# Kernel optimization log

Hardware: AMD Instinct MI355X
Metric: run time of the kernel (lower is better)

The kernel has to match this reference:

```python
import jax, jax.numpy as jnp
import numpy as np

GRID_SIZE = 2
AREA_SPAN = 1.6
EPS = 0.01
N = 4096
HIDDEN = 64
NUM_SCENES = 64


def setup_inputs() -> dict:
    key = jax.random.key(0)
    k1, k2, k3 = jax.random.split(key, 3)
    ht = jax.random.normal(k1, (N, 1, HIDDEN), dtype=jnp.float32)
    pos_t = jax.random.normal(k2, (N, 1, 2), dtype=jnp.float32)
    same_scene_mask = jnp.sort(
        jax.random.randint(k3, (N, 1), 0, NUM_SCENES, dtype=jnp.int64), axis=0
    )
    return {"ht": ht, "pos_t": pos_t, "same_scene_mask": same_scene_mask}


def reference(ht, pos_t, same_scene_mask):
    # ht: (N,1,H), pos_t: (N,1,2), same_scene_mask: (N,1) sorted scene ids
    n = ht.shape[0]
    h = ht.shape[2]
    G = GRID_SIZE * GRID_SIZE
    half = AREA_SPAN / 2.0
    cell = AREA_SPAN / GRID_SIZE

    pos = pos_t[:, 0, :]                       # (N,2)
    # rel[i,j] = pos[j] - pos[i]  (matches transpose(repeat) - repeat in torch)
    rel = pos[None, :, :] - pos[:, None, :]    # (N,N,2)

    within = (
        (rel[:, :, 0] < half - EPS) & (rel[:, :, 0] > -half + EPS)
        & (rel[:, :, 1] < half - EPS) & (rel[:, :, 1] > -half + EPS)
    )
    scene = same_scene_mask[:, 0]
    same_scene = scene[:, None] == scene[None, :]
    not_self = ~jnp.eye(n, dtype=bool)
    valid = (within & same_scene & not_self).astype(jnp.float32)  # (N,N)

    gid2 = jnp.floor((rel + half) / cell)      # (N,N,2)
    gid = gid2[:, :, 0] * GRID_SIZE + gid2[:, :, 1]
    gid = (gid * valid).astype(jnp.int32)      # invalid pairs -> bin 0 with 0 weight

    # per-pair one-hot bin weight, zeroed for invalid pairs: (N,N,G)
    w = jax.nn.one_hot(gid, G, dtype=jnp.float32) * valid[:, :, None]
    # pooled[i,g,h] = sum_j w[i,j,g] * ht[j,h]
    pooled = jnp.einsum("ijg,jh->igh", w, ht[:, 0, :])
    return pooled  # (N, G, H)
```

## Files before the change

kernel.cpp:

```cpp
#include <hip/hip_runtime.h>
#include <hip/hip_bf16.h>


#define GRID_G 4
#define HALF   0.8f
#define CELL   0.8f
#define EPSV   0.01f

__global__ __launch_bounds__(64) void social_pool_kernel(
    const float* __restrict__ ht,
    const float* __restrict__ pos,
    const int*   __restrict__ scene,
    float*       __restrict__ out,
    int n, int hidden)
{
    const int i = blockIdx.x;
    const int h = threadIdx.x;

    const int   s  = scene[i];
    const float px = pos[2 * i + 0];
    const float py = pos[2 * i + 1];

    int lo = 0, hi = n;
    while (lo < hi) {
        int mid = (lo + hi) >> 1;
        if (scene[mid] < s) lo = mid + 1; else hi = mid;
    }
    const int start = lo;
    hi = n;
    while (lo < hi) {
        int mid = (lo + hi) >> 1;
        if (scene[mid] <= s) lo = mid + 1; else hi = mid;
    }
    const int end = lo;

    float acc0 = 0.f, acc1 = 0.f, acc2 = 0.f, acc3 = 0.f;

    const float hi_b = HALF - EPSV;
    const float lo_b = -HALF + EPSV;

    for (int j = start; j < end; ++j) {
        if (j == i) continue;
        const float rx = pos[2 * j + 0] - px;
        const float ry = pos[2 * j + 1] - py;
        if (!(rx < hi_b && rx > lo_b && ry < hi_b && ry > lo_b)) continue;
        const int gx = (int)floorf((rx + HALF) / CELL);
        const int gy = (int)floorf((ry + HALF) / CELL);
        const int g  = gx * 2 + gy;
        const float v = ht[(long)j * hidden + h];
        if      (g == 0) acc0 += v;
        else if (g == 1) acc1 += v;
        else if (g == 2) acc2 += v;
        else             acc3 += v;
    }

    float* o = out + (long)i * GRID_G * hidden + h;
    o[0 * hidden] = acc0;
    o[1 * hidden] = acc1;
    o[2 * hidden] = acc2;
    o[3 * hidden] = acc3;
}

extern "C" void kernel_launch(void* const* d_in, const int* in_sizes, int n_in,
                              void* d_out, int out_size, void* d_ws, size_t ws_size,
                              hipStream_t stream)
{
    const float* ht    = (const float*)d_in[0];
    const float* pos   = (const float*)d_in[1];
    const int*   scene = (const int*)d_in[2];
    float*       out   = (float*)d_out;

    const int n      = in_sizes[2];
    const int hidden = in_sizes[0] / n;

    social_pool_kernel<<<n, hidden, 0, stream>>>(ht, pos, scene, out, n, hidden);
}
```

Measured before the change: 23.78 us.

## Precompute scene bounds in a pre-pass and use branchless quadrant accumulation

```diff
diff --git a/kernel.cpp b/kernel.cpp
--- a/kernel.cpp
+++ b/kernel.cpp
@@ -2,76 +2,89 @@
 #include <hip/hip_bf16.h>
 
 
-#define GRID_G 4
-#define HALF   0.8f
-#define CELL   0.8f
-#define EPSV   0.01f
+#define NUM_SCENES 64
+#define HI_B  0.79f
+#define LO_B -0.79f
 
-__global__ __launch_bounds__(64) void social_pool_kernel(
-    const float* __restrict__ ht,
-    const float* __restrict__ pos,
-    const int*   __restrict__ scene,
-    float*       __restrict__ out,
-    int n, int hidden)
+__global__ void scene_bounds_kernel(const int* __restrict__ scene,
+                                    int* __restrict__ starts,
+                                    int* __restrict__ ends, int n)
 {
-    const int i = blockIdx.x;
-    const int h = threadIdx.x;
+    int k = blockIdx.x * blockDim.x + threadIdx.x;
+    if (k >= n) return;
+    int s = scene[k];
+    if (k == 0) {
+        starts[s] = 0;
+    } else {
+        int sp = scene[k - 1];
+        if (sp != s) { starts[s] = k; ends[sp] = k; }
+    }
+    if (k == n - 1) ends[s] = n;
+}
 
-    const int   s  = scene[i];
-    const float px = pos[2 * i + 0];
-    const float py = pos[2 * i + 1];
+__global__ __launch_bounds__(256) void social_pool_kernel(
+    const float*  __restrict__ ht,
+    const float2* __restrict__ pos,
+    const int*    __restrict__ scene,
+    const int*    __restrict__ starts,
+    const int*    __restrict__ ends,
+    float*        __restrict__ out,
+    int n)
+{
+    const int wave = threadIdx.x >> 6;
+    const int h    = threadIdx.x & 63;
+    const int i    = blockIdx.x * 4 + wave;
+    if (i >= n) return;
 
-    int lo = 0, hi = n;
-    while (lo < hi) {
-        int mid = (lo + hi) >> 1;
-        if (scene[mid] < s) lo = mid + 1; else hi = mid;
-    }
-    const int start = lo;
-    hi = n;
-    while (lo < hi) {
-        int mid = (lo + hi) >> 1;
-        if (scene[mid] <= s) lo = mid + 1; else hi = mid;
-    }
-    const int end = lo;
+    const int s     = scene[i];
+    const int start = starts[s];
+    const int end   = ends[s];
+
+    const float2 p  = pos[i];
+    const float  px = p.x, py = p.y;
 
     float acc0 = 0.f, acc1 = 0.f, acc2 = 0.f, acc3 = 0.f;
 
-    const float hi_b = HALF - EPSV;
-    const float lo_b = -HALF + EPSV;
+    #pragma unroll 4
+    for (int j = start; j < end; ++j) {
+        const float2 q  = pos[j];
+        const float  rx = q.x - px;
+        const float  ry = q.y - py;
+        const float  v  = ht[j * 64 + h];
 
-    for (int j = start; j < end; ++j) {
-        if (j == i) continue;
-        const float rx = pos[2 * j + 0] - px;
-        const float ry = pos[2 * j + 1] - py;
-        if (!(rx < hi_b && rx > lo_b && ry < hi_b && ry > lo_b)) continue;
-        const int gx = (int)floorf((rx + HALF) / CELL);
-        const int gy = (int)floorf((ry + HALF) / CELL);
-        const int g  = gx * 2 + gy;
-        const float v = ht[(long)j * hidden + h];
-        if      (g == 0) acc0 += v;
-        else if (g == 1) acc1 += v;
-        else if (g == 2) acc2 += v;
-        else             acc3 += v;
+        const bool in = (rx < HI_B) && (rx > LO_B) &&
+                        (ry < HI_B) && (ry > LO_B) && (j != i);
+        const float vv = in ? v : 0.f;
+        const bool xp = rx >= 0.f;
+        const bool yp = ry >= 0.f;
+
+        acc0 += (!xp && !yp) ? vv : 0.f;
+        acc1 += (!xp &&  yp) ? vv : 0.f;
+        acc2 += ( xp && !yp) ? vv : 0.f;
+        acc3 += ( xp &&  yp) ? vv : 0.f;
     }
 
-    float* o = out + (long)i * GRID_G * hidden + h;
-    o[0 * hidden] = acc0;
-    o[1 * hidden] = acc1;
-    o[2 * hidden] = acc2;
-    o[3 * hidden] = acc3;
+    float* o = out + (long)i * 4 * 64 + h;
+    o[0 * 64] = acc0;
+    o[1 * 64] = acc1;
+    o[2 * 64] = acc2;
+    o[3 * 64] = acc3;
 }
 
 extern "C" void kernel_launch(void* const* d_in, const int* in_sizes, int n_in,
                               void* d_out, int out_size, void* d_ws, size_t ws_size,
                               hipStream_t stream)
 {
-    const float* ht    = (const float*)d_in[0];
-    const float* pos   = (const float*)d_in[1];
-    const int*   scene = (const int*)d_in[2];
-    float*       out   = (float*)d_out;
+    const float*  ht    = (const float*)d_in[0];
+    const float2* pos   = (const float2*)d_in[1];
+    const int*    scene = (const int*)d_in[2];
+    float*        out   = (float*)d_out;
 
-    const int n      = in_sizes[2];
-    const int hidden = in_sizes[0] / n;
+    const int n = in_sizes[2];
 
-    social_pool_kernel<<<n, hidden, 0, stream>>>(ht, pos, scene, out, n, hidden);
+    int* starts = (int*)d_ws;
+    int* ends   = starts + NUM_SCENES;
+
+    scene_bounds_kernel<<<(n + 255) / 256, 256, 0, stream>>>(scene, starts, ends, n);
+    social_pool_kernel<<<(n + 3) / 4, 256, 0, stream>>>(ht, pos, scene, starts, ends, out, n);
 }
```

Result: slower. 27.66 us (+16.3%).
